# Performance work log

Measured on AMD Instinct MI355X. Metric: run time of the kernel, lower is better.

Reference implementation:

```python
import jax, jax.numpy as jnp
import numpy as np

H = 64
N_TYPES = 20
EDGE_DIM = 4
N_GRAPHS = 128
N_LAYERS = 3
N_NODES = 50000
N_EDGES = 800000
NQ = 4

# ---- quantum-circuit constants (4 qubits, statevector of 16) ----
def _cnot_mat(c, t, n=NQ):
    m = np.zeros((2**n, 2**n), np.complex64)
    for i in range(2**n):
        bits = [(i >> (n - 1 - k)) & 1 for k in range(n)]
        jb = list(bits)
        if bits[c]:
            jb[t] ^= 1
        j = sum(b << (n - 1 - k) for k, b in enumerate(jb))
        m[j, i] = 1.0
    return m

CNOTS = jnp.array(np.stack([_cnot_mat(q, (q + 1) % NQ) for q in range(NQ)]))
ZSIGN = jnp.array(np.array([[1.0 - 2.0 * ((i >> (NQ - 1 - q)) & 1) for i in range(2**NQ)] for q in range(NQ)], np.float32))
I2 = np.eye(2, dtype=np.complex64)

def _rx(t):
    c = jnp.cos(t / 2).astype(jnp.complex64)
    s = jnp.sin(t / 2).astype(jnp.complex64)
    return jnp.stack([jnp.stack([c, -1j * s]), jnp.stack([-1j * s, c])])

def _ry(t):
    c = jnp.cos(t / 2)
    s = jnp.sin(t / 2)
    return jnp.stack([jnp.stack([c, -s]), jnp.stack([s, c])]).astype(jnp.complex64)

def _full1q(g, q):
    ops = [jnp.asarray(I2)] * NQ
    ops[q] = g
    m = ops[0]
    for o in ops[1:]:
        m = jnp.kron(m, o)
    return m

def _circuit(x, w):
    # x: [4] input angles, w: [n_layers=2, 4] RY weights
    psi = jnp.zeros(2**NQ, jnp.complex64).at[0].set(1.0)
    for q in range(NQ):
        psi = _full1q(_rx(x[q]), q) @ psi
    for l in range(w.shape[0]):
        for q in range(NQ):
            psi = _full1q(_ry(w[l, q]), q) @ psi
        for q in range(NQ):
            psi = CNOTS[q] @ psi
    probs = jnp.abs(psi) ** 2
    return ZSIGN @ probs  # PauliZ expval per qubit, [4]

def _forward(node_types, edge_index, batch, pos, edge_attr, emb, ew1, eb1, ew2, eb2,
             cw1, cb1, cw2, cb2, nw1, nb1, nw2, nb2, prew, preb, qw, pw1, pb1, pw2, pb2):
    silu = jax.nn.silu
    n = pos.shape[0]
    src, dst = edge_index[0], edge_index[1]
    deg = jnp.maximum(jax.ops.segment_sum(jnp.ones((src.shape[0],), pos.dtype), dst, num_segments=n), 1.0)[:, None]
    h = emb[node_types]  # [N, H]
    for l in range(N_LAYERS):
        rel = pos[dst] - pos[src]                      # [E, 3]
        d2 = jnp.sum(rel * rel, axis=-1, keepdims=True)  # [E, 1]
        m_in = jnp.concatenate([h[dst], h[src], d2, edge_attr], axis=-1)  # [E, 2H+1+edge_dim]
        m = silu(m_in @ ew1[l] + eb1[l])
        m = silu(m @ ew2[l] + eb2[l])                  # [E, H] messages
        c = silu(m @ cw1[l] + cb1[l]) @ cw2[l] + cb2[l]  # [E, 1] coord scalar
        pos = pos + jax.ops.segment_sum(rel * c, dst, num_segments=n) / deg
        agg = jax.ops.segment_sum(m, dst, num_segments=n)  # [N, H]
        h = h + silu(jnp.concatenate([h, agg], axis=-1) @ nw1[l] + nb1[l]) @ nw2[l] + nb2[l]
    # global mean pool over graphs
    cnt = jnp.maximum(jax.ops.segment_sum(jnp.ones((n,), h.dtype), batch, num_segments=N_GRAPHS), 1.0)[:, None]
    g = jax.ops.segment_sum(h, batch, num_segments=N_GRAPHS) / cnt  # [G, H]
    q_in = g @ prew + preb                              # [G, 4]
    q_out = jax.vmap(lambda x: _circuit(x, qw))(q_in)   # [G, 4]
    return silu(q_out @ pw1 + pb1) @ pw2 + pb2          # [G, 1]

def setup_inputs() -> dict:
    key = jax.random.key(0)
    ks = jax.random.split(key, 20)
    def lin(k, i, o, layers=None):
        shape = (i, o) if layers is None else (layers, i, o)
        return (jax.random.normal(k, shape, jnp.float32) / np.sqrt(i))
    return {
        "node_types": jax.random.randint(ks[0], (N_NODES,), 0, N_TYPES),
        "pos": jax.random.normal(ks[1], (N_NODES, 3), jnp.float32),
        "edge_index": jax.random.randint(ks[2], (2, N_EDGES), 0, N_NODES),
        "edge_attr": jax.random.normal(ks[3], (N_EDGES, EDGE_DIM), jnp.float32),
        "batch": jnp.sort(jax.random.randint(ks[4], (N_NODES,), 0, N_GRAPHS)),
        "emb": jax.random.normal(ks[5], (N_TYPES, H), jnp.float32),
        "ew1": lin(ks[6], 2 * H + 1 + EDGE_DIM, H, N_LAYERS), "eb1": jnp.zeros((N_LAYERS, H), jnp.float32),
        "ew2": lin(ks[7], H, H, N_LAYERS), "eb2": jnp.zeros((N_LAYERS, H), jnp.float32),
        "cw1": lin(ks[8], H, H, N_LAYERS), "cb1": jnp.zeros((N_LAYERS, H), jnp.float32),
        "cw2": lin(ks[9], H, 1, N_LAYERS) * 0.1, "cb2": jnp.zeros((N_LAYERS, 1), jnp.float32),
        "nw1": lin(ks[10], 2 * H, H, N_LAYERS), "nb1": jnp.zeros((N_LAYERS, H), jnp.float32),
        "nw2": lin(ks[11], H, H, N_LAYERS), "nb2": jnp.zeros((N_LAYERS, H), jnp.float32),
        "prew": lin(ks[12], H, NQ), "preb": jnp.zeros((NQ,), jnp.float32),
        "qw": jax.random.uniform(ks[13], (2, NQ), jnp.float32, 0.0, 2.0 * np.pi),
        "pw1": lin(ks[14], NQ, H), "pb1": jnp.zeros((H,), jnp.float32),
        "pw2": lin(ks[15], H, 1), "pb2": jnp.zeros((1,), jnp.float32),
    }

def reference(node_types, pos, edge_index, edge_attr, batch, emb, ew1, eb1, ew2, eb2,
              cw1, cb1, cw2, cb2, nw1, nb1, nw2, nb2, prew, preb, qw, pw1, pb1, pw2, pb2):
    return _forward(node_types, edge_index, batch, pos, edge_attr, emb, ew1, eb1, ew2, eb2,
                    cw1, cb1, cw2, cb2, nw1, nb1, nw2, nb2, prew, preb, qw, pw1, pb1, pw2, pb2)
```

## Files before the change

kernel.cpp:

```cpp
#include <hip/hip_runtime.h>

#define NN 50000
#define NE 800000
#define NG 128
#define NL 3
#define NPAIR (NE / 32)

typedef __attribute__((ext_vector_type(8))) short short8;
typedef __attribute__((ext_vector_type(4))) float f32x4;
typedef __attribute__((ext_vector_type(4))) int i32x4;

union FragU { i32x4 i; short8 s; };

__device__ __forceinline__ float silu_f(float x) { return x / (1.f + __expf(-x)); }
__device__ __forceinline__ float rdl(float v, int l) {
  return __int_as_float(__builtin_amdgcn_readlane(__float_as_int(v), l));
}
__device__ __forceinline__ float wave_sum(float v) {
#pragma unroll
  for (int m = 1; m < 64; m <<= 1) v += __shfl_xor(v, m, 64);
  return v;
}

__device__ __forceinline__ unsigned f2u(float x) { return __float_as_uint(x); }
__device__ __forceinline__ float hi_part(float x) {
  return __uint_as_float(f2u(x) & 0xffff0000u);
}
__device__ __forceinline__ unsigned pk_hi(float e0, float e1) {
  return __builtin_amdgcn_perm(f2u(e1), f2u(e0), 0x07060302u);
}

__device__ __forceinline__ f32x4 mfma16(i32x4 a, i32x4 b, f32x4 c) {
  FragU ua, ub; ua.i = a; ub.i = b;
  return __builtin_amdgcn_mfma_f32_16x16x32_bf16(ua.s, ub.s, c, 0, 0, 0);
}

__device__ __forceinline__ void split8(const float* x, i32x4& fh, i32x4& fl) {
#pragma unroll
  for (int i = 0; i < 4; ++i) {
    const float a = x[2 * i], b = x[2 * i + 1];
    fh[i] = (int)pk_hi(a, b);
    fl[i] = (int)pk_hi(a - hi_part(a), b - hi_part(b));
  }
}

__device__ __forceinline__ void wfrag(const float* __restrict__ W, int nrows, int k0,
                                      int n, int lane, i32x4& fh, i32x4& fl) {
  const int kb = k0 + ((lane >> 4) << 3);
  float x[8];
#pragma unroll
  for (int j = 0; j < 8; ++j) {
    const int k = kb + j;
    x[j] = (k < nrows) ? W[k * 64 + n] : 0.f;
  }
  split8(x, fh, fl);
}

__global__ __launch_bounds__(256) void k_init_h(const int* __restrict__ nt,
                                                const float* __restrict__ emb,
                                                float* __restrict__ h,
                                                unsigned short* __restrict__ hpk) {
  int idx = blockIdx.x * 256 + threadIdx.x;
  if (idx < NN * 64) {
    const int node = idx >> 6, c = idx & 63;
    const float v = emb[nt[node] * 64 + c];
    h[idx] = v;
    const unsigned hb = f2u(v) & 0xffff0000u;
    const float lo = v - __uint_as_float(hb);
    hpk[node * 128 + c] = (unsigned short)(hb >> 16);
    hpk[node * 128 + 64 + c] = (unsigned short)(f2u(lo) >> 16);
  }
}

__global__ __launch_bounds__(256) void k_prep(const float* __restrict__ pos_in,
                                              float* __restrict__ pos,
                                              float* __restrict__ deg,
                                              float* __restrict__ g,
                                              float* __restrict__ gcnt) {
  int idx = blockIdx.x * 256 + threadIdx.x;
  if (idx < NN * 3) pos[idx] = pos_in[idx];
  if (idx < NN) deg[idx] = 0.f;
  if (idx < NG * 64) g[idx] = 0.f;
  if (idx < NG) gcnt[idx] = 0.f;
}

__global__ __launch_bounds__(256) void k_hist(const int* __restrict__ ei,
                                              float* __restrict__ deg) {
  int e = blockIdx.x * 256 + threadIdx.x;
  if (e < NE) atomicAdd(&deg[ei[NE + e]], 1.f);
}

__global__ __launch_bounds__(256) void k_cnt(const int* __restrict__ batch,
                                             float* __restrict__ deg,
                                             float* __restrict__ gcnt) {
  int i = blockIdx.x * 256 + threadIdx.x;
  if (i < NN) {
    deg[i] = fmaxf(deg[i], 1.f);
    atomicAdd(&gcnt[batch[i]], 1.f);
  }
}

__global__ __launch_bounds__(256) void k_zero(float* __restrict__ agg,
                                              float* __restrict__ posd) {
  int idx = blockIdx.x * 256 + threadIdx.x;
  if (idx < NN * 64) agg[idx] = 0.f;
  else if (idx < NN * 64 + NN * 3) posd[idx - NN * 64] = 0.f;
}

__global__ __launch_bounds__(256) void k_pos(float* __restrict__ pos,
                                             const float* __restrict__ posd,
                                             const float* __restrict__ deg) {
  int idx = blockIdx.x * 256 + threadIdx.x;
  if (idx < NN * 3) pos[idx] += posd[idx] / deg[idx / 3];
}

__global__ __launch_bounds__(256) void k_pool(const float* __restrict__ h,
                                              const int* __restrict__ batch,
                                              float* __restrict__ g) {
  const int lane = threadIdx.x & 63;
  const int wid = (blockIdx.x * 256 + threadIdx.x) >> 6;
  const int nw = (gridDim.x * 256) >> 6;
  for (int n0 = wid * 16; n0 < NN; n0 += nw * 16) {
    float acc = 0.f;
    int curb = batch[n0];
#pragma unroll
    for (int i = 0; i < 16; ++i) {
      const int b = batch[n0 + i];
      const float v = h[(size_t)(n0 + i) * 64 + lane];
      if (b != curb) {
        atomicAdd(&g[curb * 64 + lane], acc);
        acc = 0.f;
        curb = b;
      }
      acc += v;
    }
    atomicAdd(&g[curb * 64 + lane], acc);
  }
}

__global__ __launch_bounds__(512, 2) void k_edge(
    const unsigned short* __restrict__ hpk, const float* __restrict__ pos,
    const int* __restrict__ ei, const float* __restrict__ eattr,
    const float* __restrict__ W1, const float* __restrict__ B1,
    const float* __restrict__ W2, const float* __restrict__ B2,
    const float* __restrict__ C1, const float* __restrict__ CB1,
    const float* __restrict__ C2, const float* __restrict__ CB2,
    float* __restrict__ agg, float* __restrict__ posd) {
  __shared__ i32x4 smem[8704];

  const int tid = threadIdx.x;
  const int lane = tid & 63;
  const int w = tid >> 6;
  const int m = lane & 15;
  const int quad = lane >> 4;

  for (int j = w; j < 36; j += 8) {
    int s, t, nrows, hb, lb;
    const float* W;
    if (j < 20)      { s = j >> 2; t = j & 3; W = W1; nrows = 133; hb = 0; lb = 1280; }
    else if (j < 28) { const int q = j - 20; s = q >> 2; t = q & 3; W = W2; nrows = 64; hb = 2560; lb = 3072; }
    else             { const int q = j - 28; s = q >> 2; t = q & 3; W = C1; nrows = 64; hb = 3584; lb = 4096; }
    i32x4 fh, fl;
    wfrag(W, nrows, 32 * s, t * 16 + m, lane, fh, fl);
    smem[hb + (s * 4 + t) * 64 + lane] = fh;
    smem[lb + (s * 4 + t) * 64 + lane] = fl;
  }
  __syncthreads();

  float eb1t[4], eb2t[4], cb1t[4], cw2t[4];
#pragma unroll
  for (int t = 0; t < 4; ++t) {
    eb1t[t] = B1[t * 16 + m];
    eb2t[t] = B2[t * 16 + m];
    cb1t[t] = CB1[t * 16 + m];
    cw2t[t] = C2[t * 16 + m];
  }
  const float cb2v = CB2[0];

  char* wb = (char*)(smem + 4608) + w * 8192;
  char* m1A = wb;
  char* m1B = wb + 4096;
  const char* hB = (const char*)hpk;

  const int gw0 = blockIdx.x * 8 + w;
  const int nwv = gridDim.x * 8;

  int esA = 0, edA = 0, esB = 0, edB = 0;
  if (gw0 < NPAIR) {
    const int b = gw0 * 32 + m;
    esA = ei[b]; edA = ei[NE + b]; esB = ei[b + 16]; edB = ei[NE + b + 16];
  }

#define STORE_PAIR(base, row, toff, v)                                        \
  {                                                                           \
    const float vp_ = __shfl_xor((v), 1, 64);                                 \
    if (!(m & 1)) {                                                           \
      const int off_ = (row) * 128 + ((((toff) + m * 2)) ^ (((row) & 7) << 4)); \
      *(unsigned*)((base) + off_) = pk_hi((v), vp_);                          \
      *(unsigned*)((base) + 2048 + off_) =                                    \
          pk_hi((v)-hi_part(v), vp_ - hi_part(vp_));                          \
    }                                                                         \
  }

  for (int g = gw0; g < NPAIR; g += nwv) {
    const int e0 = g * 32;
    const int cesA = esA, cedA = edA, cesB = esB, cedB = edB;
    const int g2 = g + nwv;
    if (g2 < NPAIR) {
      const int b = g2 * 32 + m;
      esA = ei[b]; edA = ei[NE + b]; esB = ei[b + 16]; edB = ei[NE + b + 16];
    }

    i32x4 fha[4], fla[4], fhb[4], flb[4];
#pragma unroll
    for (int s = 0; s < 4; ++s) {
      const unsigned node = (unsigned)(s < 2 ? cedA : cesA);
      const unsigned off = node * 256u + (unsigned)((s & 1) * 64 + quad * 16);
      fha[s] = *(const i32x4*)(hB + off);
      fla[s] = *(const i32x4*)(hB + off + 128);
    }
#pragma unroll
    for (int s = 0; s < 4; ++s) {
      const unsigned node = (unsigned)(s < 2 ? cedB : cesB);
      const unsigned off = node * 256u + (unsigned)((s & 1) * 64 + quad * 16);
      fhb[s] = *(const i32x4*)(hB + off);
      flb[s] = *(const i32x4*)(hB + off + 128);
    }

    float rx = 0.f, ry = 0.f, rz = 0.f, d2v = 0.f;
    float ea0 = 0.f, ea1 = 0.f, ea2 = 0.f, ea3 = 0.f;
    if (lane < 32) {
      const int s_ = (lane < 16) ? cesA : cesB;
      const int d_ = (lane < 16) ? cedA : cedB;
      rx = pos[d_ * 3 + 0] - pos[s_ * 3 + 0];
      ry = pos[d_ * 3 + 1] - pos[s_ * 3 + 1];
      rz = pos[d_ * 3 + 2] - pos[s_ * 3 + 2];
      d2v = rx * rx + ry * ry + rz * rz;
      const float4 ea = *(const float4*)(eattr + 4 * (e0 + lane));
      ea0 = ea.x; ea1 = ea.y; ea2 = ea.z; ea3 = ea.w;
    }

    i32x4 thA, tlA, thB, tlB;
    {
      float x0 = __shfl(d2v, m), x1 = __shfl(ea0, m), x2 = __shfl(ea1, m),
            x3 = __shfl(ea2, m), x4 = __shfl(ea3, m);
      if (quad) { x0 = x1 = x2 = x3 = x4 = 0.f; }
      float xa[8] = {x0, x1, x2, x3, x4, 0.f, 0.f, 0.f};
      split8(xa, thA, tlA);
    }
    {
      float x0 = __shfl(d2v, 16 + m), x1 = __shfl(ea0, 16 + m), x2 = __shfl(ea1, 16 + m),
            x3 = __shfl(ea2, 16 + m), x4 = __shfl(ea3, 16 + m);
      if (quad) { x0 = x1 = x2 = x3 = x4 = 0.f; }
      float xb[8] = {x0, x1, x2, x3, x4, 0.f, 0.f, 0.f};
      split8(xb, thB, tlB);
    }

#pragma unroll
    for (int t = 0; t < 4; ++t) {
      f32x4 PA = {eb1t[t], eb1t[t], eb1t[t], eb1t[t]}, QA = {0.f, 0.f, 0.f, 0.f};
      f32x4 PB = {eb1t[t], eb1t[t], eb1t[t], eb1t[t]}, QB = {0.f, 0.f, 0.f, 0.f};
#pragma unroll
      for (int s = 0; s < 4; ++s) {
        const i32x4 wh = smem[(s * 4 + t) * 64 + lane];
        const i32x4 wl = smem[1280 + (s * 4 + t) * 64 + lane];
        PA = mfma16(fha[s], wh, PA);
        QA = mfma16(fha[s], wl, QA);
        QA = mfma16(fla[s], wh, QA);
        PB = mfma16(fhb[s], wh, PB);
        QB = mfma16(fhb[s], wl, QB);
        QB = mfma16(flb[s], wh, QB);
      }
      {
        const i32x4 wh = smem[(16 + t) * 64 + lane];
        const i32x4 wl = smem[1280 + (16 + t) * 64 + lane];
        PA = mfma16(thA, wh, PA);
        QA = mfma16(thA, wl, QA);
        QA = mfma16(tlA, wh, QA);
        PB = mfma16(thB, wh, PB);
        QB = mfma16(thB, wl, QB);
        QB = mfma16(tlB, wh, QB);
      }
#pragma unroll
      for (int r = 0; r < 4; ++r) {
        const int row = quad * 4 + r;
        const float vA = silu_f(PA[r] + QA[r]);
        const float vB = silu_f(PB[r] + QB[r]);
        STORE_PAIR(m1A, row, t * 32, vA);
        STORE_PAIR(m1B, row, t * 32, vB);
      }
    }

    int rdA[4], rdB[4];
#pragma unroll
    for (int r = 0; r < 4; ++r) {
      rdA[r] = __shfl(cedA, quad * 4 + r, 64);
      rdB[r] = __shfl(cedB, quad * 4 + r, 64);
    }

    i32x4 a1hA[2], a1lA[2], a1hB[2], a1lB[2];
#pragma unroll
    for (int s = 0; s < 2; ++s) {
      const int off = m * 128 + ((s * 64 + quad * 16) ^ ((m & 7) << 4));
      a1hA[s] = *(const i32x4*)(m1A + off);
      a1lA[s] = *(const i32x4*)(m1A + 2048 + off);
      a1hB[s] = *(const i32x4*)(m1B + off);
      a1lB[s] = *(const i32x4*)(m1B + 2048 + off);
    }
#pragma unroll
    for (int t = 0; t < 4; ++t) {
      f32x4 PA = {eb2t[t], eb2t[t], eb2t[t], eb2t[t]}, QA = {0.f, 0.f, 0.f, 0.f};
      f32x4 PB = {eb2t[t], eb2t[t], eb2t[t], eb2t[t]}, QB = {0.f, 0.f, 0.f, 0.f};
#pragma unroll
      for (int s = 0; s < 2; ++s) {
        const i32x4 wh = smem[2560 + (s * 4 + t) * 64 + lane];
        const i32x4 wl = smem[3072 + (s * 4 + t) * 64 + lane];
        PA = mfma16(a1hA[s], wh, PA);
        QA = mfma16(a1hA[s], wl, QA);
        QA = mfma16(a1lA[s], wh, QA);
        PB = mfma16(a1hB[s], wh, PB);
        QB = mfma16(a1hB[s], wl, QB);
        QB = mfma16(a1lB[s], wh, QB);
      }
#pragma unroll
      for (int r = 0; r < 4; ++r) {
        const int row = quad * 4 + r;
        const float mA = silu_f(PA[r] + QA[r]);
        const float mB = silu_f(PB[r] + QB[r]);
        STORE_PAIR(m1A, row, t * 32, mA);
        STORE_PAIR(m1B, row, t * 32, mB);
        atomicAdd(&agg[(size_t)rdA[r] * 64 + t * 16 + m], mA);
        atomicAdd(&agg[(size_t)rdB[r] * 64 + t * 16 + m], mB);
      }
    }

    i32x4 mhA[2], mlA[2], mhB[2], mlB[2];
#pragma unroll
    for (int s = 0; s < 2; ++s) {
      const int off = m * 128 + ((s * 64 + quad * 16) ^ ((m & 7) << 4));
      mhA[s] = *(const i32x4*)(m1A + off);
      mlA[s] = *(const i32x4*)(m1A + 2048 + off);
      mhB[s] = *(const i32x4*)(m1B + off);
      mlB[s] = *(const i32x4*)(m1B + 2048 + off);
    }
    float trA[4] = {0.f, 0.f, 0.f, 0.f}, trB[4] = {0.f, 0.f, 0.f, 0.f};
#pragma unroll
    for (int t = 0; t < 4; ++t) {
      f32x4 PA = {cb1t[t], cb1t[t], cb1t[t], cb1t[t]}, QA = {0.f, 0.f, 0.f, 0.f};
      f32x4 PB = {cb1t[t], cb1t[t], cb1t[t], cb1t[t]}, QB = {0.f, 0.f, 0.f, 0.f};
#pragma unroll
      for (int s = 0; s < 2; ++s) {
        const i32x4 wh = smem[3584 + (s * 4 + t) * 64 + lane];
        const i32x4 wl = smem[4096 + (s * 4 + t) * 64 + lane];
        PA = mfma16(mhA[s], wh, PA);
        QA = mfma16(mhA[s], wl, QA);
        QA = mfma16(mlA[s], wh, QA);
        PB = mfma16(mhB[s], wh, PB);
        QB = mfma16(mhB[s], wl, QB);
        QB = mfma16(mlB[s], wh, QB);
      }
#pragma unroll
      for (int r = 0; r < 4; ++r) {
        trA[r] += silu_f(PA[r] + QA[r]) * cw2t[t];
        trB[r] += silu_f(PB[r] + QB[r]) * cw2t[t];
      }
    }
#pragma unroll
    for (int mask = 1; mask < 16; mask <<= 1)
#pragma unroll
      for (int r = 0; r < 4; ++r) {
        trA[r] += __shfl_xor(trA[r], mask, 64);
        trB[r] += __shfl_xor(trB[r], mask, 64);
      }
    {
      const int rr = m >> 2, cc = m & 3;
      const int e = quad * 4 + rr;
      const float tA = ((rr & 2) ? ((rr & 1) ? trA[3] : trA[2])
                                 : ((rr & 1) ? trA[1] : trA[0])) + cb2v;
      const float tB = ((rr & 2) ? ((rr & 1) ? trB[3] : trB[2])
                                 : ((rr & 1) ? trB[1] : trB[0])) + cb2v;
      const int dA_ = __shfl(cedA, e, 64);
      const int dB_ = __shfl(cedB, e, 64);
      const float axA = __shfl(rx, e, 64), ayA = __shfl(ry, e, 64), azA = __shfl(rz, e, 64);
      const float axB = __shfl(rx, 16 + e, 64), ayB = __shfl(ry, 16 + e, 64), azB = __shfl(rz, 16 + e, 64);
      if (cc < 3) {
        const float relA = cc == 0 ? axA : (cc == 1 ? ayA : azA);
        const float relB = cc == 0 ? axB : (cc == 1 ? ayB : azB);
        atomicAdd(&posd[dA_ * 3 + cc], relA * tA);
        atomicAdd(&posd[dB_ * 3 + cc], relB * tB);
      }
    }
  }
#undef STORE_PAIR
}

__global__ __launch_bounds__(256) void k_node(
    float* __restrict__ h, unsigned short* __restrict__ hpk,
    const float* __restrict__ agg,
    const float* __restrict__ W1, const float* __restrict__ B1,
    const float* __restrict__ W2, const float* __restrict__ B2) {
  __shared__ float sW1[128 * 64];
  __shared__ float sW2[64 * 64];
  for (int i = threadIdx.x; i < 128 * 64; i += 256) sW1[i] = W1[i];
  for (int i = threadIdx.x; i < 64 * 64; i += 256) sW2[i] = W2[i];
  __syncthreads();
  const int lane = threadIdx.x & 63;
  const float nb1 = B1[lane], nb2 = B2[lane];
  const int wid = (blockIdx.x * 256 + threadIdx.x) >> 6;
  const int nw = (gridDim.x * 256) >> 6;
  for (int n0 = wid * 8; n0 < NN; n0 += nw * 8) {
    float hj[8], aj[8], a1[8];
#pragma unroll
    for (int i = 0; i < 8; ++i) {
      hj[i] = h[(size_t)(n0 + i) * 64 + lane];
      aj[i] = agg[(size_t)(n0 + i) * 64 + lane];
      a1[i] = nb1;
    }
#pragma unroll
    for (int k = 0; k < 64; ++k) {
      const float wv = sW1[k * 64 + lane];
#pragma unroll
      for (int i = 0; i < 8; ++i) a1[i] += rdl(hj[i], k) * wv;
    }
#pragma unroll
    for (int k = 0; k < 64; ++k) {
      const float wv = sW1[(64 + k) * 64 + lane];
#pragma unroll
      for (int i = 0; i < 8; ++i) a1[i] += rdl(aj[i], k) * wv;
    }
    float u[8], a2[8];
#pragma unroll
    for (int i = 0; i < 8; ++i) { u[i] = silu_f(a1[i]); a2[i] = nb2; }
#pragma unroll
    for (int k = 0; k < 64; ++k) {
      const float wv = sW2[k * 64 + lane];
#pragma unroll
      for (int i = 0; i < 8; ++i) a2[i] += rdl(u[i], k) * wv;
    }
#pragma unroll
    for (int i = 0; i < 8; ++i) {
      const float hn = hj[i] + a2[i];
      h[(size_t)(n0 + i) * 64 + lane] = hn;
      const unsigned hb = f2u(hn) & 0xffff0000u;
      const float lo = hn - __uint_as_float(hb);
      hpk[(size_t)(n0 + i) * 128 + lane] = (unsigned short)(hb >> 16);
      hpk[(size_t)(n0 + i) * 128 + 64 + lane] = (unsigned short)(f2u(lo) >> 16);
    }
  }
}

__global__ __launch_bounds__(256) void k_final(
    const float* __restrict__ g, const float* __restrict__ gcnt,
    const float* __restrict__ prew, const float* __restrict__ preb,
    const float* __restrict__ qw, const float* __restrict__ pw1,
    const float* __restrict__ pb1, const float* __restrict__ pw2,
    const float* __restrict__ pb2, float* __restrict__ out) {
  const int lane = threadIdx.x & 63;
  const int gid = (blockIdx.x * 256 + threadIdx.x) >> 6;
  if (gid >= NG) return;
  const float cnt = fmaxf(gcnt[gid], 1.f);
  const float gv = g[gid * 64 + lane] / cnt;
  float qin[4];
#pragma unroll
  for (int q = 0; q < 4; ++q)
    qin[q] = wave_sum(gv * prew[lane * 4 + q]) + preb[q];
  float sr[16], si[16];
#pragma unroll
  for (int i = 0; i < 16; ++i) { sr[i] = 0.f; si[i] = 0.f; }
  sr[0] = 1.f;
#pragma unroll
  for (int q = 0; q < 4; ++q) {
    const int mask = 8 >> q;
    float s, c;
    __sincosf(qin[q] * 0.5f, &s, &c);
#pragma unroll
    for (int i = 0; i < 16; ++i)
      if (!(i & mask)) {
        const int j = i | mask;
        const float ar = sr[i], ai = si[i], br = sr[j], bi = si[j];
        sr[i] = c * ar + s * bi; si[i] = c * ai - s * br;
        sr[j] = c * br + s * ai; si[j] = c * bi - s * ar;
      }
  }
#pragma unroll
  for (int l = 0; l < 2; ++l) {
#pragma unroll
    for (int q = 0; q < 4; ++q) {
      const int mask = 8 >> q;
      float s, c;
      __sincosf(qw[l * 4 + q] * 0.5f, &s, &c);
#pragma unroll
      for (int i = 0; i < 16; ++i)
        if (!(i & mask)) {
          const int j = i | mask;
          const float ar = sr[i], ai = si[i], br = sr[j], bi = si[j];
          sr[i] = c * ar - s * br; si[i] = c * ai - s * bi;
          sr[j] = s * ar + c * br; si[j] = s * ai + c * bi;
        }
    }
#pragma unroll
    for (int q = 0; q < 4; ++q) {
      const int mc = 8 >> q;
      const int mt = 8 >> ((q + 1) & 3);
#pragma unroll
      for (int i = 0; i < 16; ++i)
        if ((i & mc) && !(i & mt)) {
          const int j = i | mt;
          float t = sr[i]; sr[i] = sr[j]; sr[j] = t;
          t = si[i]; si[i] = si[j]; si[j] = t;
        }
    }
  }
  float qo[4] = {0.f, 0.f, 0.f, 0.f};
#pragma unroll
  for (int i = 0; i < 16; ++i) {
    const float p = sr[i] * sr[i] + si[i] * si[i];
#pragma unroll
    for (int q = 0; q < 4; ++q) qo[q] += ((i >> (3 - q)) & 1) ? -p : p;
  }
  float t = pb1[lane];
#pragma unroll
  for (int q = 0; q < 4; ++q) t += qo[q] * pw1[q * 64 + lane];
  const float r = wave_sum(silu_f(t) * pw2[lane]);
  if (lane == 0) out[gid] = r + pb2[0];
}

extern "C" void kernel_launch(void* const* d_in, const int* in_sizes, int n_in,
                              void* d_out, int out_size, void* d_ws, size_t ws_size,
                              hipStream_t stream) {
  (void)in_sizes; (void)n_in; (void)out_size; (void)ws_size;
  const int*   nt    = (const int*)d_in[0];
  const float* pos0  = (const float*)d_in[1];
  const int*   ei    = (const int*)d_in[2];
  const float* eattr = (const float*)d_in[3];
  const int*   batch = (const int*)d_in[4];
  const float* emb   = (const float*)d_in[5];
  const float* ew1   = (const float*)d_in[6];
  const float* eb1   = (const float*)d_in[7];
  const float* ew2   = (const float*)d_in[8];
  const float* eb2   = (const float*)d_in[9];
  const float* cw1   = (const float*)d_in[10];
  const float* cb1   = (const float*)d_in[11];
  const float* cw2   = (const float*)d_in[12];
  const float* cb2   = (const float*)d_in[13];
  const float* nw1   = (const float*)d_in[14];
  const float* nb1   = (const float*)d_in[15];
  const float* nw2   = (const float*)d_in[16];
  const float* nb2   = (const float*)d_in[17];
  const float* prew  = (const float*)d_in[18];
  const float* preb  = (const float*)d_in[19];
  const float* qw    = (const float*)d_in[20];
  const float* pw1   = (const float*)d_in[21];
  const float* pb1   = (const float*)d_in[22];
  const float* pw2   = (const float*)d_in[23];
  const float* pb2   = (const float*)d_in[24];
  float* out = (float*)d_out;

  float* ws   = (float*)d_ws;
  float* h    = ws;
  float* pos  = h + NN * 64;
  float* posd = pos + NN * 3;
  float* agg  = posd + NN * 3;
  float* deg  = agg + NN * 64;
  float* g    = deg + NN;
  float* gcnt = g + NG * 64;
  unsigned short* hpk = (unsigned short*)(gcnt + NG);

  k_init_h<<<(NN * 64 + 255) / 256, 256, 0, stream>>>(nt, emb, h, hpk);
  k_prep<<<(NN * 3 + 255) / 256, 256, 0, stream>>>(pos0, pos, deg, g, gcnt);
  k_hist<<<(NE + 255) / 256, 256, 0, stream>>>(ei, deg);
  k_cnt<<<(NN + 255) / 256, 256, 0, stream>>>(batch, deg, gcnt);
  for (int l = 0; l < NL; ++l) {
    k_zero<<<(NN * 67 + 255) / 256, 256, 0, stream>>>(agg, posd);
    k_edge<<<256, 512, 0, stream>>>(hpk, pos, ei, eattr,
        ew1 + l * 133 * 64, eb1 + l * 64, ew2 + l * 64 * 64, eb2 + l * 64,
        cw1 + l * 64 * 64, cb1 + l * 64, cw2 + l * 64, cb2 + l, agg, posd);
    k_pos<<<(NN * 3 + 255) / 256, 256, 0, stream>>>(pos, posd, deg);
    k_node<<<512, 256, 0, stream>>>(h, hpk, agg, nw1 + l * 128 * 64, nb1 + l * 64,
                                    nw2 + l * 64 * 64, nb2 + l * 64);
  }
  k_pool<<<800, 256, 0, stream>>>(h, batch, g);
  k_final<<<(NG * 64 + 255) / 256, 256, 0, stream>>>(g, gcnt, prew, preb, qw,
                                                     pw1, pb1, pw2, pb2, out);
}
```

Measured before the change: 1.240 ms.

## Process one 16-edge group per wave with 16 waves per block; fold zeroing into consumers

```diff
diff --git a/kernel.cpp b/kernel.cpp
--- a/kernel.cpp
+++ b/kernel.cpp
@@ -4,7 +4,7 @@
 #define NE 800000
 #define NG 128
 #define NL 3
-#define NPAIR (NE / 32)
+#define NGRP (NE / 16)
 
 typedef __attribute__((ext_vector_type(8))) short short8;
 typedef __attribute__((ext_vector_type(4))) float f32x4;
@@ -76,9 +76,12 @@
                                               float* __restrict__ pos,
                                               float* __restrict__ deg,
                                               float* __restrict__ g,
-                                              float* __restrict__ gcnt) {
+                                              float* __restrict__ gcnt,
+                                              float* __restrict__ agg,
+                                              float* __restrict__ posd) {
   int idx = blockIdx.x * 256 + threadIdx.x;
-  if (idx < NN * 3) pos[idx] = pos_in[idx];
+  if (idx < NN * 64) agg[idx] = 0.f;
+  if (idx < NN * 3) { pos[idx] = pos_in[idx]; posd[idx] = 0.f; }
   if (idx < NN) deg[idx] = 0.f;
   if (idx < NG * 64) g[idx] = 0.f;
   if (idx < NG) gcnt[idx] = 0.f;
@@ -100,18 +103,14 @@
   }
 }
 
-__global__ __launch_bounds__(256) void k_zero(float* __restrict__ agg,
-                                              float* __restrict__ posd) {
-  int idx = blockIdx.x * 256 + threadIdx.x;
-  if (idx < NN * 64) agg[idx] = 0.f;
-  else if (idx < NN * 64 + NN * 3) posd[idx - NN * 64] = 0.f;
-}
-
 __global__ __launch_bounds__(256) void k_pos(float* __restrict__ pos,
-                                             const float* __restrict__ posd,
+                                             float* __restrict__ posd,
                                              const float* __restrict__ deg) {
   int idx = blockIdx.x * 256 + threadIdx.x;
-  if (idx < NN * 3) pos[idx] += posd[idx] / deg[idx / 3];
+  if (idx < NN * 3) {
+    pos[idx] += posd[idx] / deg[idx / 3];
+    posd[idx] = 0.f;
+  }
 }
 
 __global__ __launch_bounds__(256) void k_pool(const float* __restrict__ h,
@@ -138,7 +137,7 @@
   }
 }
 
-__global__ __launch_bounds__(512, 2) void k_edge(
+__global__ __launch_bounds__(1024, 4) void k_edge(
     const unsigned short* __restrict__ hpk, const float* __restrict__ pos,
     const int* __restrict__ ei, const float* __restrict__ eattr,
     const float* __restrict__ W1, const float* __restrict__ B1,
@@ -154,7 +153,7 @@
   const int m = lane & 15;
   const int quad = lane >> 4;
 
-  for (int j = w; j < 36; j += 8) {
+  for (int j = w; j < 36; j += 16) {
     int s, t, nrows, hb, lb;
     const float* W;
     if (j < 20)      { s = j >> 2; t = j & 3; W = W1; nrows = 133; hb = 0; lb = 1280; }
@@ -177,217 +176,162 @@
   }
   const float cb2v = CB2[0];
 
-  char* wb = (char*)(smem + 4608) + w * 8192;
-  char* m1A = wb;
-  char* m1B = wb + 4096;
+  char* pl = (char*)(smem + 4608) + w * 4096;
   const char* hB = (const char*)hpk;
 
-  const int gw0 = blockIdx.x * 8 + w;
-  const int nwv = gridDim.x * 8;
-
-  int esA = 0, edA = 0, esB = 0, edB = 0;
-  if (gw0 < NPAIR) {
-    const int b = gw0 * 32 + m;
-    esA = ei[b]; edA = ei[NE + b]; esB = ei[b + 16]; edB = ei[NE + b + 16];
-  }
-
-#define STORE_PAIR(base, row, toff, v)                                        \
-  {                                                                           \
-    const float vp_ = __shfl_xor((v), 1, 64);                                 \
-    if (!(m & 1)) {                                                           \
+  const int gw0 = blockIdx.x * 16 + w;
+  const int nwv = gridDim.x * 16;
+
+  int es = 0, ed = 0;
+  if (gw0 < NGRP) {
+    es = ei[gw0 * 16 + m];
+    ed = ei[NE + gw0 * 16 + m];
+  }
+
+#define STORE_PAIR(base, row, toff, v)                                          \
+  {                                                                             \
+    const float vp_ = __shfl_xor((v), 1, 64);                                   \
+    if (!(m & 1)) {                                                             \
       const int off_ = (row) * 128 + ((((toff) + m * 2)) ^ (((row) & 7) << 4)); \
-      *(unsigned*)((base) + off_) = pk_hi((v), vp_);                          \
-      *(unsigned*)((base) + 2048 + off_) =                                    \
-          pk_hi((v)-hi_part(v), vp_ - hi_part(vp_));                          \
-    }                                                                         \
-  }
-
-  for (int g = gw0; g < NPAIR; g += nwv) {
-    const int e0 = g * 32;
-    const int cesA = esA, cedA = edA, cesB = esB, cedB = edB;
+      *(unsigned*)((base) + off_) = pk_hi((v), vp_);                            \
+      *(unsigned*)((base) + 2048 + off_) =                                      \
+          pk_hi((v)-hi_part(v), vp_ - hi_part(vp_));                            \
+    }                                                                           \
+  }
+
+  for (int g = gw0; g < NGRP; g += nwv) {
+    const int e0 = g * 16;
+    const int ces = es, ced = ed;
     const int g2 = g + nwv;
-    if (g2 < NPAIR) {
-      const int b = g2 * 32 + m;
-      esA = ei[b]; edA = ei[NE + b]; esB = ei[b + 16]; edB = ei[NE + b + 16];
-    }
-
-    i32x4 fha[4], fla[4], fhb[4], flb[4];
+    if (g2 < NGRP) {
+      es = ei[g2 * 16 + m];
+      ed = ei[NE + g2 * 16 + m];
+    }
+
+    i32x4 fh[4], fl[4];
 #pragma unroll
     for (int s = 0; s < 4; ++s) {
-      const unsigned node = (unsigned)(s < 2 ? cedA : cesA);
+      const unsigned node = (unsigned)(s < 2 ? ced : ces);
       const unsigned off = node * 256u + (unsigned)((s & 1) * 64 + quad * 16);
-      fha[s] = *(const i32x4*)(hB + off);
-      fla[s] = *(const i32x4*)(hB + off + 128);
-    }
-#pragma unroll
-    for (int s = 0; s < 4; ++s) {
-      const unsigned node = (unsigned)(s < 2 ? cedB : cesB);
-      const unsigned off = node * 256u + (unsigned)((s & 1) * 64 + quad * 16);
-      fhb[s] = *(const i32x4*)(hB + off);
-      flb[s] = *(const i32x4*)(hB + off + 128);
+      fh[s] = *(const i32x4*)(hB + off);
+      fl[s] = *(const i32x4*)(hB + off + 128);
     }
 
     float rx = 0.f, ry = 0.f, rz = 0.f, d2v = 0.f;
     float ea0 = 0.f, ea1 = 0.f, ea2 = 0.f, ea3 = 0.f;
-    if (lane < 32) {
-      const int s_ = (lane < 16) ? cesA : cesB;
-      const int d_ = (lane < 16) ? cedA : cedB;
-      rx = pos[d_ * 3 + 0] - pos[s_ * 3 + 0];
-      ry = pos[d_ * 3 + 1] - pos[s_ * 3 + 1];
-      rz = pos[d_ * 3 + 2] - pos[s_ * 3 + 2];
+    if (lane < 16) {
+      rx = pos[ced * 3 + 0] - pos[ces * 3 + 0];
+      ry = pos[ced * 3 + 1] - pos[ces * 3 + 1];
+      rz = pos[ced * 3 + 2] - pos[ces * 3 + 2];
       d2v = rx * rx + ry * ry + rz * rz;
       const float4 ea = *(const float4*)(eattr + 4 * (e0 + lane));
       ea0 = ea.x; ea1 = ea.y; ea2 = ea.z; ea3 = ea.w;
     }
 
-    i32x4 thA, tlA, thB, tlB;
+    i32x4 th, tl;
     {
       float x0 = __shfl(d2v, m), x1 = __shfl(ea0, m), x2 = __shfl(ea1, m),
             x3 = __shfl(ea2, m), x4 = __shfl(ea3, m);
       if (quad) { x0 = x1 = x2 = x3 = x4 = 0.f; }
-      float xa[8] = {x0, x1, x2, x3, x4, 0.f, 0.f, 0.f};
-      split8(xa, thA, tlA);
-    }
-    {
-      float x0 = __shfl(d2v, 16 + m), x1 = __shfl(ea0, 16 + m), x2 = __shfl(ea1, 16 + m),
-            x3 = __shfl(ea2, 16 + m), x4 = __shfl(ea3, 16 + m);
-      if (quad) { x0 = x1 = x2 = x3 = x4 = 0.f; }
-      float xb[8] = {x0, x1, x2, x3, x4, 0.f, 0.f, 0.f};
-      split8(xb, thB, tlB);
+      float xt[8] = {x0, x1, x2, x3, x4, 0.f, 0.f, 0.f};
+      split8(xt, th, tl);
     }
 
 #pragma unroll
     for (int t = 0; t < 4; ++t) {
-      f32x4 PA = {eb1t[t], eb1t[t], eb1t[t], eb1t[t]}, QA = {0.f, 0.f, 0.f, 0.f};
-      f32x4 PB = {eb1t[t], eb1t[t], eb1t[t], eb1t[t]}, QB = {0.f, 0.f, 0.f, 0.f};
+      f32x4 P = {eb1t[t], eb1t[t], eb1t[t], eb1t[t]}, Q = {0.f, 0.f, 0.f, 0.f};
 #pragma unroll
       for (int s = 0; s < 4; ++s) {
         const i32x4 wh = smem[(s * 4 + t) * 64 + lane];
         const i32x4 wl = smem[1280 + (s * 4 + t) * 64 + lane];
-        PA = mfma16(fha[s], wh, PA);
-        QA = mfma16(fha[s], wl, QA);
-        QA = mfma16(fla[s], wh, QA);
-        PB = mfma16(fhb[s], wh, PB);
-        QB = mfma16(fhb[s], wl, QB);
-        QB = mfma16(flb[s], wh, QB);
+        P = mfma16(fh[s], wh, P);
+        Q = mfma16(fh[s], wl, Q);
+        Q = mfma16(fl[s], wh, Q);
       }
       {
         const i32x4 wh = smem[(16 + t) * 64 + lane];
         const i32x4 wl = smem[1280 + (16 + t) * 64 + lane];
-        PA = mfma16(thA, wh, PA);
-        QA = mfma16(thA, wl, QA);
-        QA = mfma16(tlA, wh, QA);
-        PB = mfma16(thB, wh, PB);
-        QB = mfma16(thB, wl, QB);
-        QB = mfma16(tlB, wh, QB);
+        P = mfma16(th, wh, P);
+        Q = mfma16(th, wl, Q);
+        Q = mfma16(tl, wh, Q);
       }
 #pragma unroll
       for (int r = 0; r < 4; ++r) {
         const int row = quad * 4 + r;
-        const float vA = silu_f(PA[r] + QA[r]);
-        const float vB = silu_f(PB[r] + QB[r]);
-        STORE_PAIR(m1A, row, t * 32, vA);
-        STORE_PAIR(m1B, row, t * 32, vB);
-      }
-    }
-
-    int rdA[4], rdB[4];
-#pragma unroll
-    for (int r = 0; r < 4; ++r) {
-      rdA[r] = __shfl(cedA, quad * 4 + r, 64);
-      rdB[r] = __shfl(cedB, quad * 4 + r, 64);
-    }
-
-    i32x4 a1hA[2], a1lA[2], a1hB[2], a1lB[2];
+        const float v = silu_f(P[r] + Q[r]);
+        STORE_PAIR(pl, row, t * 32, v);
+      }
+    }
+
+    int rd[4];
+#pragma unroll
+    for (int r = 0; r < 4; ++r) rd[r] = __shfl(ced, quad * 4 + r, 64);
+
+    i32x4 ah[2], al[2];
 #pragma unroll
     for (int s = 0; s < 2; ++s) {
       const int off = m * 128 + ((s * 64 + quad * 16) ^ ((m & 7) << 4));
-      a1hA[s] = *(const i32x4*)(m1A + off);
-      a1lA[s] = *(const i32x4*)(m1A + 2048 + off);
-      a1hB[s] = *(const i32x4*)(m1B + off);
-      a1lB[s] = *(const i32x4*)(m1B + 2048 + off);
+      ah[s] = *(const i32x4*)(pl + off);
+      al[s] = *(const i32x4*)(pl + 2048 + off);
     }
 #pragma unroll
     for (int t = 0; t < 4; ++t) {
-      f32x4 PA = {eb2t[t], eb2t[t], eb2t[t], eb2t[t]}, QA = {0.f, 0.f, 0.f, 0.f};
-      f32x4 PB = {eb2t[t], eb2t[t], eb2t[t], eb2t[t]}, QB = {0.f, 0.f, 0.f, 0.f};
+      f32x4 P = {eb2t[t], eb2t[t], eb2t[t], eb2t[t]}, Q = {0.f, 0.f, 0.f, 0.f};
 #pragma unroll
       for (int s = 0; s < 2; ++s) {
         const i32x4 wh = smem[2560 + (s * 4 + t) * 64 + lane];
         const i32x4 wl = smem[3072 + (s * 4 + t) * 64 + lane];
-        PA = mfma16(a1hA[s], wh, PA);
-        QA = mfma16(a1hA[s], wl, QA);
-        QA = mfma16(a1lA[s], wh, QA);
-        PB = mfma16(a1hB[s], wh, PB);
-        QB = mfma16(a1hB[s], wl, QB);
-        QB = mfma16(a1lB[s], wh, QB);
+        P = mfma16(ah[s], wh, P);
+        Q = mfma16(ah[s], wl, Q);
+        Q = mfma16(al[s], wh, Q);
       }
 #pragma unroll
       for (int r = 0; r < 4; ++r) {
         const int row = quad * 4 + r;
-        const float mA = silu_f(PA[r] + QA[r]);
-        const float mB = silu_f(PB[r] + QB[r]);
-        STORE_PAIR(m1A, row, t * 32, mA);
-        STORE_PAIR(m1B, row, t * 32, mB);
-        atomicAdd(&agg[(size_t)rdA[r] * 64 + t * 16 + m], mA);
-        atomicAdd(&agg[(size_t)rdB[r] * 64 + t * 16 + m], mB);
-      }
-    }
-
-    i32x4 mhA[2], mlA[2], mhB[2], mlB[2];
+        const float mv = silu_f(P[r] + Q[r]);
+        STORE_PAIR(pl, row, t * 32, mv);
+        atomicAdd(&agg[(size_t)rd[r] * 64 + t * 16 + m], mv);
+      }
+    }
+
+    i32x4 mh[2], ml[2];
 #pragma unroll
     for (int s = 0; s < 2; ++s) {
       const int off = m * 128 + ((s * 64 + quad * 16) ^ ((m & 7) << 4));
-      mhA[s] = *(const i32x4*)(m1A + off);
-      mlA[s] = *(const i32x4*)(m1A + 2048 + off);
-      mhB[s] = *(const i32x4*)(m1B + off);
-      mlB[s] = *(const i32x4*)(m1B + 2048 + off);
-    }
-    float trA[4] = {0.f, 0.f, 0.f, 0.f}, trB[4] = {0.f, 0.f, 0.f, 0.f};
+      mh[s] = *(const i32x4*)(pl + off);
+      ml[s] = *(const i32x4*)(pl + 2048 + off);
+    }
+    float tr[4] = {0.f, 0.f, 0.f, 0.f};
 #pragma unroll
     for (int t = 0; t < 4; ++t) {
-      f32x4 PA = {cb1t[t], cb1t[t], cb1t[t], cb1t[t]}, QA = {0.f, 0.f, 0.f, 0.f};
-      f32x4 PB = {cb1t[t], cb1t[t], cb1t[t], cb1t[t]}, QB = {0.f, 0.f, 0.f, 0.f};
+      f32x4 P = {cb1t[t], cb1t[t], cb1t[t], cb1t[t]}, Q = {0.f, 0.f, 0.f, 0.f};
 #pragma unroll
       for (int s = 0; s < 2; ++s) {
         const i32x4 wh = smem[3584 + (s * 4 + t) * 64 + lane];
         const i32x4 wl = smem[4096 + (s * 4 + t) * 64 + lane];
-        PA = mfma16(mhA[s], wh, PA);
-        QA = mfma16(mhA[s], wl, QA);
-        QA = mfma16(mlA[s], wh, QA);
-        PB = mfma16(mhB[s], wh, PB);
-        QB = mfma16(mhB[s], wl, QB);
-        QB = mfma16(mlB[s], wh, QB);
-      }
-#pragma unroll
-      for (int r = 0; r < 4; ++r) {
-        trA[r] += silu_f(PA[r] + QA[r]) * cw2t[t];
-        trB[r] += silu_f(PB[r] + QB[r]) * cw2t[t];
-      }
+        P = mfma16(mh[s], wh, P);
+        Q = mfma16(mh[s], wl, Q);
+        Q = mfma16(ml[s], wh, Q);
+      }
+#pragma unroll
+      for (int r = 0; r < 4; ++r) tr[r] += silu_f(P[r] + Q[r]) * cw2t[t];
     }
 #pragma unroll
     for (int mask = 1; mask < 16; mask <<= 1)
 #pragma unroll
-      for (int r = 0; r < 4; ++r) {
-        trA[r] += __shfl_xor(trA[r], mask, 64);
-        trB[r] += __shfl_xor(trB[r], mask, 64);
-      }
+      for (int r = 0; r < 4; ++r) tr[r] += __shfl_xor(tr[r], mask, 64);
+
     {
       const int rr = m >> 2, cc = m & 3;
       const int e = quad * 4 + rr;
-      const float tA = ((rr & 2) ? ((rr & 1) ? trA[3] : trA[2])
-                                 : ((rr & 1) ? trA[1] : trA[0])) + cb2v;
-      const float tB = ((rr & 2) ? ((rr & 1) ? trB[3] : trB[2])
-                                 : ((rr & 1) ? trB[1] : trB[0])) + cb2v;
-      const int dA_ = __shfl(cedA, e, 64);
-      const int dB_ = __shfl(cedB, e, 64);
-      const float axA = __shfl(rx, e, 64), ayA = __shfl(ry, e, 64), azA = __shfl(rz, e, 64);
-      const float axB = __shfl(rx, 16 + e, 64), ayB = __shfl(ry, 16 + e, 64), azB = __shfl(rz, 16 + e, 64);
+      const float tv = ((rr & 2) ? ((rr & 1) ? tr[3] : tr[2])
+                                 : ((rr & 1) ? tr[1] : tr[0])) + cb2v;
+      const int d_ = __shfl(ced, e, 64);
+      const float ax = __shfl(rx, e, 64), ay = __shfl(ry, e, 64),
+                  az = __shfl(rz, e, 64);
       if (cc < 3) {
-        const float relA = cc == 0 ? axA : (cc == 1 ? ayA : azA);
-        const float relB = cc == 0 ? axB : (cc == 1 ? ayB : azB);
-        atomicAdd(&posd[dA_ * 3 + cc], relA * tA);
-        atomicAdd(&posd[dB_ * 3 + cc], relB * tB);
+        const float rel = cc == 0 ? ax : (cc == 1 ? ay : az);
+        atomicAdd(&posd[d_ * 3 + cc], rel * tv);
       }
     }
   }
@@ -396,7 +340,7 @@
 
 __global__ __launch_bounds__(256) void k_node(
     float* __restrict__ h, unsigned short* __restrict__ hpk,
-    const float* __restrict__ agg,
+    float* __restrict__ agg,
     const float* __restrict__ W1, const float* __restrict__ B1,
     const float* __restrict__ W2, const float* __restrict__ B2) {
   __shared__ float sW1[128 * 64];
@@ -416,6 +360,8 @@
       aj[i] = agg[(size_t)(n0 + i) * 64 + lane];
       a1[i] = nb1;
     }
+#pragma unroll
+    for (int i = 0; i < 8; ++i) agg[(size_t)(n0 + i) * 64 + lane] = 0.f;
 #pragma unroll
     for (int k = 0; k < 64; ++k) {
       const float wv = sW1[k * 64 + lane];
@@ -567,12 +513,12 @@
   unsigned short* hpk = (unsigned short*)(gcnt + NG);
 
   k_init_h<<<(NN * 64 + 255) / 256, 256, 0, stream>>>(nt, emb, h, hpk);
-  k_prep<<<(NN * 3 + 255) / 256, 256, 0, stream>>>(pos0, pos, deg, g, gcnt);
+  k_prep<<<(NN * 64 + 255) / 256, 256, 0, stream>>>(pos0, pos, deg, g, gcnt,
+                                                    agg, posd);
   k_hist<<<(NE + 255) / 256, 256, 0, stream>>>(ei, deg);
   k_cnt<<<(NN + 255) / 256, 256, 0, stream>>>(batch, deg, gcnt);
   for (int l = 0; l < NL; ++l) {
-    k_zero<<<(NN * 67 + 255) / 256, 256, 0, stream>>>(agg, posd);
-    k_edge<<<256, 512, 0, stream>>>(hpk, pos, ei, eattr,
+    k_edge<<<256, 1024, 0, stream>>>(hpk, pos, ei, eattr,
         ew1 + l * 133 * 64, eb1 + l * 64, ew2 + l * 64 * 64, eb2 + l * 64,
         cw1 + l * 64 * 64, cb1 + l * 64, cw2 + l * 64, cb2 + l, agg, posd);
     k_pos<<<(NN * 3 + 255) / 256, 256, 0, stream>>>(pos, posd, deg);
```

Result: slower. 1.350 ms (+8.9%).
